# Performance work log

Measured on AMD Instinct MI355X. Metric: run time of the kernel, lower is better.

Reference implementation:

```python
import jax, jax.numpy as jnp
import numpy as np
import math

B, S, D, H = 2, 2048, 1024, 16
DK = D // H


def setup_inputs() -> dict:
    key = jax.random.key(0)
    ks = jax.random.split(key, 8)
    s = 1.0 / math.sqrt(D)
    inp = {
        "query": jax.random.normal(ks[0], (B, S, D), jnp.float32),
        "key": jax.random.normal(ks[1], (B, S, D), jnp.float32),
        "value": jax.random.normal(ks[2], (B, S, D), jnp.float32),
        # causal mask: (1, 1, S, S), 1 where attention allowed
        "mask": jnp.tril(jnp.ones((S, S), jnp.int32))[None, None, :, :],
        "Wq": jax.random.normal(ks[3], (D, D), jnp.float32) * s,
        "Wk": jax.random.normal(ks[4], (D, D), jnp.float32) * s,
        "Wv": jax.random.normal(ks[5], (D, D), jnp.float32) * s,
        "Wo": jax.random.normal(ks[6], (D, D), jnp.float32) * s,
    }
    return inp


def reference(query, key, value, mask, Wq, Wk, Wv, Wo):
    # nn.Linear(bias=False): y = x @ W.T
    def proj_heads(x, W):
        y = jnp.einsum("bsd,ed->bse", x, W)          # (B,S,D)
        return y.reshape(B, -1, H, DK).transpose(0, 2, 1, 3)  # (B,H,S,DK)

    q = proj_heads(query, Wq)
    k = proj_heads(key, Wk)
    v = proj_heads(value, Wv)

    scale = jnp.asarray(math.sqrt(DK), q.dtype)
    scores = jnp.einsum("bhqd,bhkd->bhqk", q, k) / scale  # (B,H,S,S)
    scores = jnp.where(mask == 0, -jnp.inf, scores)
    attn = jax.nn.softmax(scores, axis=-1)
    # dropout p=0.0 (eval): identity
    out = jnp.einsum("bhqk,bhkd->bhqd", attn, v)          # (B,H,S,DK)
    concat = out.transpose(0, 2, 1, 3).reshape(B, -1, D)  # (B,S,D)
    return jnp.einsum("bsd,ed->bse", concat, Wo)
```

## Files before the change

### kernel.cpp

```cpp
#include <hip/hip_runtime.h>
#include <hip/hip_bf16.h>

#define B_ 2
#define S_ 2048
#define D_ 1024
#define H_ 16
#define DK_ 64

typedef __hip_bfloat16 bf16;
typedef __attribute__((ext_vector_type(8))) short bf16x8;
typedef __attribute__((ext_vector_type(4))) short bf16x4;
typedef __attribute__((ext_vector_type(4))) float f32x4;

#define GLDS16(g, l)                                                     \
    __builtin_amdgcn_global_load_lds(                                    \
        (const __attribute__((address_space(1))) void*)(g),              \
        (__attribute__((address_space(3))) void*)(l), 16, 0, 0)

#define MFMA_K32(a, b, c) __builtin_amdgcn_mfma_f32_16x16x32_bf16(a, b, c, 0, 0, 0)
#define MFMA_K16(a, b, c) __builtin_amdgcn_mfma_f32_16x16x16bf16_1k(a, b, c, 0, 0, 0)
#define EXP2F(x) __builtin_amdgcn_exp2f(x)

__global__ __launch_bounds__(256) void cvt_all(
    const float* __restrict__ q, const float* __restrict__ k, const float* __restrict__ v,
    const float* __restrict__ w0, const float* __restrict__ w1,
    const float* __restrict__ w2, const float* __restrict__ w3,
    bf16* __restrict__ oq, bf16* __restrict__ ok, bf16* __restrict__ ov,
    bf16* __restrict__ o0, bf16* __restrict__ o1, bf16* __restrict__ o2,
    bf16* __restrict__ o3) {
    int bid = blockIdx.x;
    const float* src; bf16* dst; int base;
    if      (bid < 2048) { src = q;  dst = oq; base = bid; }
    else if (bid < 4096) { src = k;  dst = ok; base = bid - 2048; }
    else if (bid < 6144) { src = v;  dst = ov; base = bid - 4096; }
    else if (bid < 6656) { src = w0; dst = o0; base = bid - 6144; }
    else if (bid < 7168) { src = w1; dst = o1; base = bid - 6656; }
    else if (bid < 7680) { src = w2; dst = o2; base = bid - 7168; }
    else                 { src = w3; dst = o3; base = bid - 7680; }
    int i = (base * 256 + threadIdx.x) * 8;
    float4 a = *(const float4*)(src + i);
    float4 b = *(const float4*)(src + i + 4);
    __align__(16) bf16 o[8];
    o[0] = __float2bfloat16(a.x); o[1] = __float2bfloat16(a.y);
    o[2] = __float2bfloat16(a.z); o[3] = __float2bfloat16(a.w);
    o[4] = __float2bfloat16(b.x); o[5] = __float2bfloat16(b.y);
    o[6] = __float2bfloat16(b.z); o[7] = __float2bfloat16(b.w);
    *(bf16x8*)(dst + i) = *(const bf16x8*)o;
}

template <int NT>
__device__ __forceinline__ void proj_loop(const bf16* __restrict__ X,
                                          const bf16* __restrict__ W,
                                          int m0, int n0, bf16* As, bf16* Bs,
                                          f32x4 (&acc)[2][NT]) {
    const int K = D_;
    const int tid = threadIdx.x;
    const int lane = tid & 63, wave = tid >> 6;
    const int lm = lane & 15, quad = lane >> 4;
    constexpr int BROWS = NT * 16;

    auto stage = [&](int t, int bf) {
        int k0 = t * 32;
        bf16* Ab = As + bf * (128 * 32);
        bf16* Bb = Bs + bf * (BROWS * 32);
#pragma unroll
        for (int i = 0; i < 2; ++i) {
            int s = i * 256 + tid;
            int row = s >> 2;
            int c = (s & 3) ^ ((row >> 1) & 3);
            GLDS16(X + (size_t)(m0 + row) * K + k0 + c * 8, Ab + s * 8);
        }
#pragma unroll
        for (int i = 0; i < NT / 4; ++i) {
            int s = i * 256 + tid;
            int row = s >> 2;
            int c = (s & 3) ^ ((row >> 1) & 3);
            GLDS16(W + (size_t)(n0 + row) * K + k0 + c * 8, Bb + s * 8);
        }
    };

    stage(0, 0);
    for (int t = 0; t < K / 32; ++t) {
        __syncthreads();
        if (t + 1 < K / 32) stage(t + 1, (t + 1) & 1);
        const bf16* Ab = As + (t & 1) * (128 * 32);
        const bf16* Bb = Bs + (t & 1) * (BROWS * 32);
        bf16x8 aF[2], bF[NT];
#pragma unroll
        for (int mt = 0; mt < 2; ++mt) {
            int row = wave * 32 + mt * 16 + lm;
            aF[mt] = *(const bf16x8*)(Ab + row * 32 + (quad ^ ((row >> 1) & 3)) * 8);
        }
#pragma unroll
        for (int nt = 0; nt < NT; ++nt) {
            int row = nt * 16 + lm;
            bF[nt] = *(const bf16x8*)(Bb + row * 32 + (quad ^ ((row >> 1) & 3)) * 8);
        }
#pragma unroll
        for (int mt = 0; mt < 2; ++mt)
#pragma unroll
            for (int nt = 0; nt < NT; ++nt)
                acc[mt][nt] = MFMA_K32(aF[mt], bF[nt], acc[mt][nt]);
    }
}

__global__ __launch_bounds__(256) void proj_qkv(
    const bf16* __restrict__ qx, const bf16* __restrict__ kx, const bf16* __restrict__ vx,
    const bf16* __restrict__ wq, const bf16* __restrict__ wk, const bf16* __restrict__ wv,
    bf16* __restrict__ qb, bf16* __restrict__ kb, bf16* __restrict__ vtb) {
    __shared__ __align__(16) bf16 As[2 * 128 * 32];
    __shared__ __align__(16) bf16 Bs[2 * 128 * 32];
    const int z = blockIdx.z;
    const bf16* X = (z == 0) ? qx : (z == 1) ? kx : vx;
    const bf16* W = (z == 0) ? wq : (z == 1) ? wk : wv;
    const int n0 = blockIdx.x * 128;
    const int m0 = blockIdx.y * 128;
    f32x4 acc[2][8] = {};
    proj_loop<8>(X, W, m0, n0, As, Bs, acc);

    const int lane = threadIdx.x & 63, wave = threadIdx.x >> 6;
    const int lm = lane & 15, quad = lane >> 4;
#pragma unroll
    for (int mt = 0; mt < 2; ++mt) {
        int mbase = m0 + wave * 32 + mt * 16 + quad * 4;
#pragma unroll
        for (int nt = 0; nt < 8; ++nt) {
            int n = n0 + nt * 16 + lm;
            if (z == 2) {
                int b = mbase >> 11, s = mbase & (S_ - 1);
                unsigned short u[4];
#pragma unroll
                for (int r = 0; r < 4; ++r) {
                    bf16 hv = __float2bfloat16(acc[mt][nt][r]);
                    u[r] = *(unsigned short*)&hv;
                }
                ushort4 pk = {u[0], u[1], u[2], u[3]};
                *(ushort4*)(vtb + ((size_t)(b * 1024 + n) * S_ + s)) = pk;
            } else {
                bf16* Y = z ? kb : qb;
#pragma unroll
                for (int r = 0; r < 4; ++r)
                    Y[(size_t)(mbase + r) * D_ + n] = __float2bfloat16(acc[mt][nt][r]);
            }
        }
    }
}

__global__ __launch_bounds__(256) void proj_o(const bf16* __restrict__ X,
                                              const bf16* __restrict__ W,
                                              float* __restrict__ Y) {
    __shared__ __align__(16) bf16 As[2 * 128 * 32];
    __shared__ __align__(16) bf16 Bs[2 * 64 * 32];
    const int n0 = blockIdx.x * 64;
    const int m0 = blockIdx.y * 128;
    f32x4 acc[2][4] = {};
    proj_loop<4>(X, W, m0, n0, As, Bs, acc);

    const int lane = threadIdx.x & 63, wave = threadIdx.x >> 6;
    const int lm = lane & 15, quad = lane >> 4;
#pragma unroll
    for (int mt = 0; mt < 2; ++mt) {
        int mbase = m0 + wave * 32 + mt * 16 + quad * 4;
#pragma unroll
        for (int nt = 0; nt < 4; ++nt) {
            int n = n0 + nt * 16 + lm;
#pragma unroll
            for (int r = 0; r < 4; ++r)
                Y[(size_t)(mbase + r) * D_ + n] = acc[mt][nt][r];
        }
    }
}

__global__ __launch_bounds__(512) void attn_kernel(const bf16* __restrict__ Q,
                                                   const bf16* __restrict__ Kb,
                                                   const bf16* __restrict__ VT,
                                                   bf16* __restrict__ O) {
    __shared__ __align__(16) bf16 kt[2][128 * 64];
    __shared__ __align__(16) bf16 vt[2][64 * 128];

    const int tid = threadIdx.x;
    const int lane = tid & 63, wave = tid >> 6;
    const int lm = lane & 15, quad = lane >> 4;
    const int qc = (int)(gridDim.x - 1 - blockIdx.x);
    const int h = blockIdx.y, b = blockIdx.z;
    const int q0 = qc * 128 + wave * 16;

    const size_t bhoff = (size_t)b * S_ * D_ + (size_t)h * DK_;
    const bf16* vtb = VT + ((size_t)b * 1024 + h * DK_) * S_;

    const bf16* qp = Q + bhoff + (size_t)(q0 + lm) * D_ + quad * 8;
    bf16x8 aq0 = *(const bf16x8*)(qp);
    bf16x8 aq1 = *(const bf16x8*)(qp + 32);

    f32x4 oacc[4] = {};
    float lsum = 0.f;
    const float cexp = 0.125f * 1.44269504f;

    auto stage = [&](int i, int bf) {
        int j0s = i * 128;
#pragma unroll
        for (int ii = 0; ii < 2; ++ii) {
            int s = ii * 512 + tid;
            int j = s >> 3, c = (s & 7) ^ (j & 7);
            GLDS16(Kb + bhoff + (size_t)(j0s + j) * D_ + c * 8, kt[bf] + s * 8);
        }
#pragma unroll
        for (int ii = 0; ii < 2; ++ii) {
            int s = ii * 512 + tid;
            int d = s >> 4, c = (s & 15) ^ (d & 15);
            GLDS16(vtb + (size_t)d * S_ + j0s + c * 8, vt[bf] + s * 8);
        }
    };

    auto chunk = [&](const bf16* ktb, const bf16* vtl, int st, bool mk) {
        int j = st * 16 + lm;
        bf16x8 bk0 = *(const bf16x8*)(ktb + (((j << 3) | (quad ^ (j & 7))) * 8));
        bf16x8 bk1 = *(const bf16x8*)(ktb + (((j << 3) | ((4 + quad) ^ (j & 7))) * 8));
        f32x4 z = {};
        z = MFMA_K32(bk0, aq0, z);
        z = MFMA_K32(bk1, aq1, z);
        bf16x4 pa;
        float rs = 0.f;
#pragma unroll
        for (int r = 0; r < 4; ++r) {
            float p = EXP2F(z[r] * cexp);
            if (mk && (quad * 4 + r > lm)) p = 0.f;
            rs += p;
            bf16 hv = __float2bfloat16(p);
            pa[r] = *(short*)&hv;
        }
        lsum += rs;
#pragma unroll
        for (int dt = 0; dt < 4; ++dt) {
            int d = dt * 16 + lm;
            int cl = st * 2 + (quad >> 1);
            bf16x4 bv = *(const bf16x4*)(vtl + d * 128 +
                                         ((cl ^ (d & 15)) * 8 + (quad & 1) * 4));
            oacc[dt] = MFMA_K16(pa, bv, oacc[dt]);
        }
    };

    stage(0, 0);

    for (int i = 0; i <= qc; ++i) {
        __syncthreads();
        if (i < qc) stage(i + 1, (i + 1) & 1);
        const bf16* ktb = kt[i & 1];
        const bf16* vtl = vt[i & 1];
        if (i < qc) {
#pragma unroll
            for (int st = 0; st < 8; ++st) chunk(ktb, vtl, st, false);
        } else {
            for (int st = 0; st < wave; ++st) chunk(ktb, vtl, st, false);
            chunk(ktb, vtl, wave, true);
        }
    }

    float l = lsum;
    l += __shfl_xor(l, 16, 64);
    l += __shfl_xor(l, 32, 64);
#pragma unroll
    for (int r = 0; r < 4; ++r) {
        float inv = 1.f / __shfl(l, quad * 4 + r, 64);
        int qrow = q0 + quad * 4 + r;
#pragma unroll
        for (int dt = 0; dt < 4; ++dt) {
            int d = dt * 16 + lm;
            O[bhoff + (size_t)qrow * D_ + d] = __float2bfloat16(oacc[dt][r] * inv);
        }
    }
}

extern "C" void kernel_launch(void* const* d_in, const int* in_sizes, int n_in,
                              void* d_out, int out_size, void* d_ws, size_t ws_size,
                              hipStream_t stream) {
    const float* q_in = (const float*)d_in[0];
    const float* k_in = (const float*)d_in[1];
    const float* v_in = (const float*)d_in[2];
    const float* Wq_f = (const float*)d_in[4];
    const float* Wk_f = (const float*)d_in[5];
    const float* Wv_f = (const float*)d_in[6];
    const float* Wo_f = (const float*)d_in[7];
    float* out = (float*)d_out;

    const size_t NEL = (size_t)B_ * S_ * D_;
    const size_t WEL = (size_t)D_ * D_;
    bf16* p = (bf16*)d_ws;
    bf16* qx = p;  p += NEL;
    bf16* kx = p;  p += NEL;
    bf16* vx = p;  p += NEL;
    bf16* wq = p;  p += WEL;
    bf16* wk = p;  p += WEL;
    bf16* wv = p;  p += WEL;
    bf16* wo = p;  p += WEL;
    bf16* qb = p;  p += NEL;
    bf16* kb = p;  p += NEL;
    bf16* vtb = p; p += NEL;
    bf16* cb = p;  p += NEL;

    cvt_all<<<8192, 256, 0, stream>>>(q_in, k_in, v_in, Wq_f, Wk_f, Wv_f, Wo_f,
                                      qx, kx, vx, wq, wk, wv, wo);

    dim3 gqkv(D_ / 128, (B_ * S_) / 128, 3);
    proj_qkv<<<gqkv, 256, 0, stream>>>(qx, kx, vx, wq, wk, wv, qb, kb, vtb);

    dim3 gattn(S_ / 128, H_, B_);
    attn_kernel<<<gattn, 512, 0, stream>>>(qb, kb, vtb, cb);

    dim3 gproj(D_ / 64, (B_ * S_) / 128);
    proj_o<<<gproj, 256, 0, stream>>>(cb, wo, out);
}
```

Before: 238.5 us.

## Split attention KV tiles across wave halves with smaller query blocks

Attention blocks now cover 64 query rows instead of 128, so the grid has twice as many blocks. Within each block, two groups of four waves process alternate 16-key sub-chunks of each 64-key tile. The partial outputs and row sums are combined through shared memory at the end. The aim is better occupancy and load balance under causal masking, at the cost of an extra reduction step and more K/V reloading across blocks.

```diff
diff --git a/kernel.cpp b/kernel.cpp
--- a/kernel.cpp
+++ b/kernel.cpp
@@ -171,19 +171,20 @@
     }
 }
 
-__global__ __launch_bounds__(512) void attn_kernel(const bf16* __restrict__ Q,
-                                                   const bf16* __restrict__ Kb,
-                                                   const bf16* __restrict__ VT,
-                                                   bf16* __restrict__ O) {
-    __shared__ __align__(16) bf16 kt[2][128 * 64];
-    __shared__ __align__(16) bf16 vt[2][64 * 128];
+__global__ __launch_bounds__(512, 8) void attn_kernel(const bf16* __restrict__ Q,
+                                                      const bf16* __restrict__ Kb,
+                                                      const bf16* __restrict__ VT,
+                                                      bf16* __restrict__ O) {
+    __shared__ __align__(16) bf16 kt[2][64 * 64];
+    __shared__ __align__(16) bf16 vt[2][64 * 64];
 
     const int tid = threadIdx.x;
     const int lane = tid & 63, wave = tid >> 6;
+    const int g = wave & 3, half = wave >> 2;
     const int lm = lane & 15, quad = lane >> 4;
-    const int qc = (int)(gridDim.x - 1 - blockIdx.x);
+    const int qi = (int)(gridDim.x - 1 - blockIdx.x);
     const int h = blockIdx.y, b = blockIdx.z;
-    const int q0 = qc * 128 + wave * 16;
+    const int q0 = qi * 64 + g * 16;
 
     const size_t bhoff = (size_t)b * S_ * D_ + (size_t)h * DK_;
     const bf16* vtb = VT + ((size_t)b * 1024 + h * DK_) * S_;
@@ -197,18 +198,14 @@
     const float cexp = 0.125f * 1.44269504f;
 
     auto stage = [&](int i, int bf) {
-        int j0s = i * 128;
-#pragma unroll
-        for (int ii = 0; ii < 2; ++ii) {
-            int s = ii * 512 + tid;
-            int j = s >> 3, c = (s & 7) ^ (j & 7);
-            GLDS16(Kb + bhoff + (size_t)(j0s + j) * D_ + c * 8, kt[bf] + s * 8);
-        }
-#pragma unroll
-        for (int ii = 0; ii < 2; ++ii) {
-            int s = ii * 512 + tid;
-            int d = s >> 4, c = (s & 15) ^ (d & 15);
-            GLDS16(vtb + (size_t)d * S_ + j0s + c * 8, vt[bf] + s * 8);
+        int j0s = i * 64;
+        {
+            int j = tid >> 3, c = (tid & 7) ^ (j & 7);
+            GLDS16(Kb + bhoff + (size_t)(j0s + j) * D_ + c * 8, kt[bf] + tid * 8);
+        }
+        {
+            int d = tid >> 3, c = (tid & 7) ^ (d & 7);
+            GLDS16(vtb + (size_t)d * S_ + j0s + c * 8, vt[bf] + tid * 8);
         }
     };
 
@@ -234,39 +231,64 @@
         for (int dt = 0; dt < 4; ++dt) {
             int d = dt * 16 + lm;
             int cl = st * 2 + (quad >> 1);
-            bf16x4 bv = *(const bf16x4*)(vtl + d * 128 +
-                                         ((cl ^ (d & 15)) * 8 + (quad & 1) * 4));
+            bf16x4 bv = *(const bf16x4*)(vtl + d * 64 +
+                                         ((cl ^ (d & 7)) * 8 + (quad & 1) * 4));
             oacc[dt] = MFMA_K16(pa, bv, oacc[dt]);
         }
     };
 
     stage(0, 0);
 
-    for (int i = 0; i <= qc; ++i) {
+    for (int i = 0; i <= qi; ++i) {
         __syncthreads();
-        if (i < qc) stage(i + 1, (i + 1) & 1);
+        if (i < qi) stage(i + 1, (i + 1) & 1);
         const bf16* ktb = kt[i & 1];
         const bf16* vtl = vt[i & 1];
-        if (i < qc) {
-#pragma unroll
-            for (int st = 0; st < 8; ++st) chunk(ktb, vtl, st, false);
+        if (i < qi) {
+            chunk(ktb, vtl, 2 * half, false);
+            chunk(ktb, vtl, 2 * half + 1, false);
         } else {
-            for (int st = 0; st < wave; ++st) chunk(ktb, vtl, st, false);
-            chunk(ktb, vtl, wave, true);
-        }
-    }
-
+#pragma unroll
+            for (int sti = 0; sti < 2; ++sti) {
+                int st = 2 * half + sti;
+                if (st < g) chunk(ktb, vtl, st, false);
+                else if (st == g) chunk(ktb, vtl, st, true);
+            }
+        }
+    }
+
+    __syncthreads();
     float l = lsum;
     l += __shfl_xor(l, 16, 64);
     l += __shfl_xor(l, 32, 64);
-#pragma unroll
-    for (int r = 0; r < 4; ++r) {
-        float inv = 1.f / __shfl(l, quad * 4 + r, 64);
-        int qrow = q0 + quad * 4 + r;
-#pragma unroll
-        for (int dt = 0; dt < 4; ++dt) {
-            int d = dt * 16 + lm;
-            O[bhoff + (size_t)qrow * D_ + d] = __float2bfloat16(oacc[dt][r] * inv);
+
+    float* scro = (float*)kt;
+    float* scrl = (float*)vt;
+    if (half == 1) {
+#pragma unroll
+        for (int dt = 0; dt < 4; ++dt)
+#pragma unroll
+            for (int r = 0; r < 4; ++r)
+                scro[((g * 4 + dt) * 4 + r) * 64 + lane] = oacc[dt][r];
+        if (quad == 0) scrl[g * 16 + lm] = l;
+    }
+    __syncthreads();
+    if (half == 0) {
+        l += scrl[g * 16 + lm];
+#pragma unroll
+        for (int dt = 0; dt < 4; ++dt)
+#pragma unroll
+            for (int r = 0; r < 4; ++r)
+                oacc[dt][r] += scro[((g * 4 + dt) * 4 + r) * 64 + lane];
+#pragma unroll
+        for (int r = 0; r < 4; ++r) {
+            float inv = 1.f / __shfl(l, quad * 4 + r, 64);
+            int qrow = q0 + quad * 4 + r;
+#pragma unroll
+            for (int dt = 0; dt < 4; ++dt) {
+                int d = dt * 16 + lm;
+                O[bhoff + (size_t)qrow * D_ + d] = __float2bfloat16(oacc[dt][r] * inv);
+            }
         }
     }
 }
@@ -304,7 +326,7 @@
     dim3 gqkv(D_ / 128, (B_ * S_) / 128, 3);
     proj_qkv<<<gqkv, 256, 0, stream>>>(qx, kx, vx, wq, wk, wv, qb, kb, vtb);
 
-    dim3 gattn(S_ / 128, H_, B_);
+    dim3 gattn(S_ / 64, H_, B_);
     attn_kernel<<<gattn, 512, 0, stream>>>(qb, kb, vtb, cb);
 
     dim3 gproj(D_ / 64, (B_ * S_) / 128);
```

Result: slower. 249.4 us (+4.6%).

## Use 64-deep K tiles and 128x64 blocks in projections; remap attention grid

Applied to the files above, without the earlier changes.

The projection GEMM loop now stages 64-wide K slices with an 8-way XOR swizzle, which halves the number of barrier iterations. The QKV projection switches from 128x128 to 128x64 output tiles, doubling its block count. The attention grid is flattened to 1D, and block indices are remapped so that the longest causal query chunks are scheduled first and neighbouring blocks spread across batch-head combos, to improve load balance and cache locality. The trade-offs are more LDS per block and less operand reuse per QKV block.

```diff
diff --git a/kernel.cpp b/kernel.cpp
--- a/kernel.cpp
+++ b/kernel.cpp
@@ -48,59 +48,60 @@
     *(bf16x8*)(dst + i) = *(const bf16x8*)o;
 }
 
-template <int NT>
-__device__ __forceinline__ void proj_loop(const bf16* __restrict__ X,
-                                          const bf16* __restrict__ W,
-                                          int m0, int n0, bf16* As, bf16* Bs,
-                                          f32x4 (&acc)[2][NT]) {
+__device__ __forceinline__ void proj_loop64(const bf16* __restrict__ X,
+                                            const bf16* __restrict__ W,
+                                            int m0, int n0, bf16* As, bf16* Bs,
+                                            f32x4 (&acc)[2][4]) {
     const int K = D_;
     const int tid = threadIdx.x;
     const int lane = tid & 63, wave = tid >> 6;
     const int lm = lane & 15, quad = lane >> 4;
-    constexpr int BROWS = NT * 16;
 
     auto stage = [&](int t, int bf) {
-        int k0 = t * 32;
-        bf16* Ab = As + bf * (128 * 32);
-        bf16* Bb = Bs + bf * (BROWS * 32);
+        int k0 = t * 64;
+        bf16* Ab = As + bf * (128 * 64);
+        bf16* Bb = Bs + bf * (64 * 64);
+#pragma unroll
+        for (int i = 0; i < 4; ++i) {
+            int s = i * 256 + tid;
+            int row = s >> 3, c = (s & 7) ^ (row & 7);
+            GLDS16(X + (size_t)(m0 + row) * K + k0 + c * 8, Ab + s * 8);
+        }
 #pragma unroll
         for (int i = 0; i < 2; ++i) {
             int s = i * 256 + tid;
-            int row = s >> 2;
-            int c = (s & 3) ^ ((row >> 1) & 3);
-            GLDS16(X + (size_t)(m0 + row) * K + k0 + c * 8, Ab + s * 8);
-        }
-#pragma unroll
-        for (int i = 0; i < NT / 4; ++i) {
-            int s = i * 256 + tid;
-            int row = s >> 2;
-            int c = (s & 3) ^ ((row >> 1) & 3);
+            int row = s >> 3, c = (s & 7) ^ (row & 7);
             GLDS16(W + (size_t)(n0 + row) * K + k0 + c * 8, Bb + s * 8);
         }
     };
 
     stage(0, 0);
-    for (int t = 0; t < K / 32; ++t) {
+    for (int t = 0; t < K / 64; ++t) {
         __syncthreads();
-        if (t + 1 < K / 32) stage(t + 1, (t + 1) & 1);
-        const bf16* Ab = As + (t & 1) * (128 * 32);
-        const bf16* Bb = Bs + (t & 1) * (BROWS * 32);
-        bf16x8 aF[2], bF[NT];
-#pragma unroll
-        for (int mt = 0; mt < 2; ++mt) {
-            int row = wave * 32 + mt * 16 + lm;
-            aF[mt] = *(const bf16x8*)(Ab + row * 32 + (quad ^ ((row >> 1) & 3)) * 8);
-        }
-#pragma unroll
-        for (int nt = 0; nt < NT; ++nt) {
-            int row = nt * 16 + lm;
-            bF[nt] = *(const bf16x8*)(Bb + row * 32 + (quad ^ ((row >> 1) & 3)) * 8);
-        }
-#pragma unroll
-        for (int mt = 0; mt < 2; ++mt)
-#pragma unroll
-            for (int nt = 0; nt < NT; ++nt)
-                acc[mt][nt] = MFMA_K32(aF[mt], bF[nt], acc[mt][nt]);
+        if (t + 1 < K / 64) stage(t + 1, (t + 1) & 1);
+        const bf16* Ab = As + (t & 1) * (128 * 64);
+        const bf16* Bb = Bs + (t & 1) * (64 * 64);
+#pragma unroll
+        for (int ks = 0; ks < 2; ++ks) {
+            bf16x8 aF[2], bF[4];
+#pragma unroll
+            for (int mt = 0; mt < 2; ++mt) {
+                int row = wave * 32 + mt * 16 + lm;
+                aF[mt] = *(const bf16x8*)(Ab + row * 64 +
+                                          ((ks * 4 + quad) ^ (row & 7)) * 8);
+            }
+#pragma unroll
+            for (int nt = 0; nt < 4; ++nt) {
+                int row = nt * 16 + lm;
+                bF[nt] = *(const bf16x8*)(Bb + row * 64 +
+                                          ((ks * 4 + quad) ^ (row & 7)) * 8);
+            }
+#pragma unroll
+            for (int mt = 0; mt < 2; ++mt)
+#pragma unroll
+                for (int nt = 0; nt < 4; ++nt)
+                    acc[mt][nt] = MFMA_K32(aF[mt], bF[nt], acc[mt][nt]);
+        }
     }
 }
 
@@ -108,15 +109,15 @@
     const bf16* __restrict__ qx, const bf16* __restrict__ kx, const bf16* __restrict__ vx,
     const bf16* __restrict__ wq, const bf16* __restrict__ wk, const bf16* __restrict__ wv,
     bf16* __restrict__ qb, bf16* __restrict__ kb, bf16* __restrict__ vtb) {
-    __shared__ __align__(16) bf16 As[2 * 128 * 32];
-    __shared__ __align__(16) bf16 Bs[2 * 128 * 32];
+    __shared__ __align__(16) bf16 As[2 * 128 * 64];
+    __shared__ __align__(16) bf16 Bs[2 * 64 * 64];
     const int z = blockIdx.z;
     const bf16* X = (z == 0) ? qx : (z == 1) ? kx : vx;
     const bf16* W = (z == 0) ? wq : (z == 1) ? wk : wv;
-    const int n0 = blockIdx.x * 128;
+    const int n0 = blockIdx.x * 64;
     const int m0 = blockIdx.y * 128;
-    f32x4 acc[2][8] = {};
-    proj_loop<8>(X, W, m0, n0, As, Bs, acc);
+    f32x4 acc[2][4] = {};
+    proj_loop64(X, W, m0, n0, As, Bs, acc);
 
     const int lane = threadIdx.x & 63, wave = threadIdx.x >> 6;
     const int lm = lane & 15, quad = lane >> 4;
@@ -124,7 +125,7 @@
     for (int mt = 0; mt < 2; ++mt) {
         int mbase = m0 + wave * 32 + mt * 16 + quad * 4;
 #pragma unroll
-        for (int nt = 0; nt < 8; ++nt) {
+        for (int nt = 0; nt < 4; ++nt) {
             int n = n0 + nt * 16 + lm;
             if (z == 2) {
                 int b = mbase >> 11, s = mbase & (S_ - 1);
@@ -149,12 +150,12 @@
 __global__ __launch_bounds__(256) void proj_o(const bf16* __restrict__ X,
                                               const bf16* __restrict__ W,
                                               float* __restrict__ Y) {
-    __shared__ __align__(16) bf16 As[2 * 128 * 32];
-    __shared__ __align__(16) bf16 Bs[2 * 64 * 32];
+    __shared__ __align__(16) bf16 As[2 * 128 * 64];
+    __shared__ __align__(16) bf16 Bs[2 * 64 * 64];
     const int n0 = blockIdx.x * 64;
     const int m0 = blockIdx.y * 128;
     f32x4 acc[2][4] = {};
-    proj_loop<4>(X, W, m0, n0, As, Bs, acc);
+    proj_loop64(X, W, m0, n0, As, Bs, acc);
 
     const int lane = threadIdx.x & 63, wave = threadIdx.x >> 6;
     const int lm = lane & 15, quad = lane >> 4;
@@ -181,9 +182,13 @@
     const int tid = threadIdx.x;
     const int lane = tid & 63, wave = tid >> 6;
     const int lm = lane & 15, quad = lane >> 4;
-    const int qc = (int)(gridDim.x - 1 - blockIdx.x);
-    const int h = blockIdx.y, b = blockIdx.z;
-    const int q0 = qc * 128 + wave * 16;
+    const int f = (int)blockIdx.x;
+    const int cls = f & 7;
+    const int t = f >> 3;
+    const int qi = 15 - (t >> 2);
+    const int combo = cls + 8 * (t & 3);
+    const int b = combo >> 4, h = combo & 15;
+    const int q0 = qi * 128 + wave * 16;
 
     const size_t bhoff = (size_t)b * S_ * D_ + (size_t)h * DK_;
     const bf16* vtb = VT + ((size_t)b * 1024 + h * DK_) * S_;
@@ -242,12 +247,12 @@
 
     stage(0, 0);
 
-    for (int i = 0; i <= qc; ++i) {
+    for (int i = 0; i <= qi; ++i) {
         __syncthreads();
-        if (i < qc) stage(i + 1, (i + 1) & 1);
+        if (i < qi) stage(i + 1, (i + 1) & 1);
         const bf16* ktb = kt[i & 1];
         const bf16* vtl = vt[i & 1];
-        if (i < qc) {
+        if (i < qi) {
 #pragma unroll
             for (int st = 0; st < 8; ++st) chunk(ktb, vtl, st, false);
         } else {
@@ -301,11 +306,10 @@
     cvt_all<<<8192, 256, 0, stream>>>(q_in, k_in, v_in, Wq_f, Wk_f, Wv_f, Wo_f,
                                       qx, kx, vx, wq, wk, wv, wo);
 
-    dim3 gqkv(D_ / 128, (B_ * S_) / 128, 3);
+    dim3 gqkv(D_ / 64, (B_ * S_) / 128, 3);
     proj_qkv<<<gqkv, 256, 0, stream>>>(qx, kx, vx, wq, wk, wv, qb, kb, vtb);
 
-    dim3 gattn(S_ / 128, H_, B_);
-    attn_kernel<<<gattn, 512, 0, stream>>>(qb, kb, vtb, cb);
+    attn_kernel<<<dim3(512), 512, 0, stream>>>(qb, kb, vtb, cb);
 
     dim3 gproj(D_ / 64, (B_ * S_) / 128);
     proj_o<<<gproj, 256, 0, stream>>>(cb, wo, out);
```

Measured after the change: 217.9 us. 8.6% less time.
